# Optimization experiments

Measured on AMD Instinct MI355X. Metric: run time of the kernel, lower is better.

## Reference

```python
import jax, jax.numpy as jnp
import numpy as np

P = 3            # spline degree
N_KNOTS = 68     # len(t); K = N_KNOTS - P - 1 = 64
B, D_IN, D_OUT = 4096, 256, 256


def bspline_basis(u, t, p):
    """Vectorized Cox-de Boor recursion.
    u: (N,) evaluation points; t: (n,) sorted knot vector.
    Returns (N, n - p - 1) basis matrix.
    """
    n = t.shape[0]
    uu = u[:, None]                                   # (N, 1)
    # degree-0 indicators over half-open knot intervals: (N, n-1)
    Bmat = ((uu >= t[None, :-1]) & (uu < t[None, 1:])).astype(u.dtype)
    for d in range(1, p + 1):
        ld = t[d:n - 1] - t[:n - d - 1]               # (n-d-1,) left denominators
        rd = t[d + 1:] - t[1:n - d]                   # (n-d-1,) right denominators
        lt = jnp.where(ld > 0, (uu - t[None, :n - d - 1]) / jnp.where(ld > 0, ld, 1.0), 0.0)
        rt = jnp.where(rd > 0, (t[None, d + 1:] - uu) / jnp.where(rd > 0, rd, 1.0), 0.0)
        Bmat = lt * Bmat[:, :-1] + rt * Bmat[:, 1:]
    return Bmat                                        # (N, K)


def setup_inputs() -> dict:
    key = jax.random.key(0)
    k1, k2 = jax.random.split(key)
    K = N_KNOTS - P - 1
    x = jax.random.normal(k1, (B, D_IN), dtype=jnp.float32)
    coeffs = 0.01 * jax.random.normal(k2, (D_OUT, D_IN, K), dtype=jnp.float32)
    mask = jnp.ones((D_OUT, D_IN), dtype=jnp.float32)
    t = jnp.linspace(-4.0, 4.0, N_KNOTS, dtype=jnp.float32)
    return {"x": x, "coeffs": coeffs, "mask": mask, "t": t}


def reference(x, coeffs, mask, t):
    b, d_in = x.shape
    # basis for all (batch, input-dim) points at once -> (B, d_in, K)
    Bx = bspline_basis(x.reshape(-1), t, P).reshape(b, d_in, -1)
    C = coeffs * mask[..., None]                      # (d_out, d_in, K)
    y = jnp.einsum('bik,oik->bo', Bx, C)              # (B, d_out)
    return y
```

## Files before the change

kernel.cpp:

```cpp
#include <hip/hip_runtime.h>

#define NKNOTS 68
#define B_     4096
#define DIN    256
#define DOUT   256
#define KB_    64
#define BM     128
#define BN     128
#define LDT    72
#define KSPLIT 8

typedef unsigned short ushort_t;
typedef __bf16 bf16_t;
typedef bf16_t  bf16x8   __attribute__((ext_vector_type(8)));
typedef float   f32x4    __attribute__((ext_vector_type(4)));
typedef unsigned int u32x4 __attribute__((ext_vector_type(4)));
typedef ushort_t us16x4  __attribute__((ext_vector_type(4)));

__device__ __forceinline__ float bf2f(ushort_t b) {
    union { unsigned u; float f; } c; c.u = ((unsigned)b) << 16; return c.f;
}
__device__ __forceinline__ ushort_t f2bf(float f) {
    union { float f; unsigned u; } c; c.f = f;
    unsigned u = c.u;
    return (ushort_t)((u + 0x7FFFu + ((u >> 16) & 1u)) >> 16);
}
__device__ __forceinline__ bool is_fp32(const void* tkn) {
    return ((*(const unsigned*)tkn) & 0xFFFFu) == 0u;
}

__global__ void kan_maskmul(const void* __restrict__ coeffs,
                            const void* __restrict__ mask,
                            const void* __restrict__ tkn,
                            ushort_t* __restrict__ cp) {
    int tid = blockIdx.x * 256 + threadIdx.x;
    int oi = tid >> 3;
    int k8 = (tid & 7) * 8;
    size_t base = (size_t)oi * KB_ + k8;
    float v[8], m;
    if (is_fp32(tkn)) {
        const float* cf = (const float*)coeffs + base;
        f32x4 a = *(const f32x4*)cf;
        f32x4 b = *(const f32x4*)(cf + 4);
        v[0] = a.x; v[1] = a.y; v[2] = a.z; v[3] = a.w;
        v[4] = b.x; v[5] = b.y; v[6] = b.z; v[7] = b.w;
        m = ((const float*)mask)[oi];
    } else {
        const ushort_t* ch = (const ushort_t*)coeffs + base;
        u32x4 w = *(const u32x4*)ch;
        const ushort_t* h = (const ushort_t*)&w;
        #pragma unroll
        for (int e = 0; e < 8; ++e) v[e] = bf2f(h[e]);
        m = bf2f(((const ushort_t*)mask)[oi]);
    }
    us16x4 o0, o1;
    #pragma unroll
    for (int e = 0; e < 4; ++e) o0[e] = f2bf(v[e] * m);
    #pragma unroll
    for (int e = 0; e < 4; ++e) o1[e] = f2bf(v[4 + e] * m);
    *(us16x4*)(cp + base)     = o0;
    *(us16x4*)(cp + base + 4) = o1;
}

__global__ void kan_basis(const void* __restrict__ x,
                          const void* __restrict__ tkn,
                          ushort_t* __restrict__ basis4,
                          unsigned char* __restrict__ span) {
    __shared__ float tt[NKNOTS];
    int lt = threadIdx.x;
    bool f32 = is_fp32(tkn);
    if (lt < NKNOTS) tt[lt] = f32 ? ((const float*)tkn)[lt] : bf2f(((const ushort_t*)tkn)[lt]);
    __syncthreads();
    int g = blockIdx.x * 256 + lt;
    float u = f32 ? ((const float*)x)[g] : bf2f(((const ushort_t*)x)[g]);
    float N0 = 0.f, N1 = 0.f, N2 = 0.f, N3 = 0.f;
    int j = 0;
    bool valid = (u >= tt[0]) && (u < tt[NKNOTS - 1]);
    if (valid) {
        int lo = 0, hi = NKNOTS - 1;
        #pragma unroll
        for (int it = 0; it < 7; ++it) {
            int mid = (lo + hi) >> 1;
            if (u < tt[mid]) hi = mid; else lo = mid;
        }
        j = lo;
        float Nv[4];
        Nv[0] = 1.f; Nv[1] = 0.f; Nv[2] = 0.f; Nv[3] = 0.f;
        #pragma unroll
        for (int d = 1; d <= 3; ++d) {
            float saved = 0.f;
            #pragma unroll
            for (int r = 0; r < 3; ++r) {
                if (r < d) {
                    int il = j + r + 1 - d;
                    int ir = j + r + 1;
                    il = il < 0 ? 0 : (il > 67 ? 67 : il);
                    ir = ir > 67 ? 67 : ir;
                    float tl = tt[il], tr = tt[ir];
                    float denom = tr - tl;
                    float temp = (denom > 0.f) ? Nv[r] / denom : 0.f;
                    Nv[r] = saved + (tr - u) * temp;
                    saved = (u - tl) * temp;
                }
            }
            Nv[d] = saved;
        }
        N0 = Nv[0]; N1 = Nv[1]; N2 = Nv[2]; N3 = Nv[3];
    }
    int s = j - 3;
    int sc = s < 0 ? 0 : (s > 60 ? 60 : s);
    us16x4 o4;
    #pragma unroll
    for (int r = 0; r < 4; ++r) {
        int rr = (sc + r) - s;
        float v = 0.f;
        v = (rr == 0) ? N0 : v;
        v = (rr == 1) ? N1 : v;
        v = (rr == 2) ? N2 : v;
        v = (rr == 3) ? N3 : v;
        o4[r] = f2bf(v);
    }
    ((us16x4*)basis4)[g] = o4;
    span[g] = (unsigned char)sc;
}

__global__ __launch_bounds__(256, 2) void kan_gemm(
    const ushort_t* __restrict__ cp,
    const ushort_t* __restrict__ basis4,
    const unsigned char* __restrict__ span,
    float* __restrict__ part)
{
    __shared__ ushort_t smem[2 * BM * LDT];
    ushort_t* As = smem;
    ushort_t* Bs = smem + BM * LDT;

    int t  = threadIdx.x;
    int bx = blockIdx.x;
    int kt = bx & 7;
    int mt = (bx >> 3) & 31;
    int nt = bx >> 8;
    int b0 = mt * BM;
    int o0 = nt * BN;
    int i0 = kt * (DIN / KSPLIT);

    int wave = t >> 6;
    int lane = t & 63;
    int wm = (wave & 1) * 64;
    int wn = (wave >> 1) * 64;
    int l15 = lane & 15;
    int l4  = lane >> 4;

    f32x4 acc[4][4];
    #pragma unroll
    for (int a = 0; a < 4; ++a)
        #pragma unroll
        for (int b = 0; b < 4; ++b)
            acc[a][b] = (f32x4){0.f, 0.f, 0.f, 0.f};

    int zrow = t >> 2;
    int zq   = t & 3;
    int brow = t >> 1;
    int bh   = t & 1;

    for (int ii = 0; ii < DIN / KSPLIT; ++ii) {
        int i = i0 + ii;
        const u32x4* gB = (const u32x4*)(cp + ((size_t)(o0 + brow) * DIN + i) * KB_ + bh * 32);
        u32x4 vb0 = gB[0], vb1 = gB[1], vb2 = gB[2], vb3 = gB[3];
        int r0g = b0 + zrow, r1g = r0g + 64;
        unsigned s0 = span[(size_t)r0g * DIN + i];
        unsigned s1 = span[(size_t)r1g * DIN + i];
        ushort_t bv0 = basis4[((size_t)r0g * DIN + i) * 4 + zq];
        ushort_t bv1 = basis4[((size_t)r1g * DIN + i) * 4 + zq];
        u32x4 z4 = (u32x4){0u, 0u, 0u, 0u};
        u32x4* az0 = (u32x4*)(As + zrow * LDT + zq * 16);
        u32x4* az1 = (u32x4*)(As + (zrow + 64) * LDT + zq * 16);
        az0[0] = z4; az0[1] = z4;
        az1[0] = z4; az1[1] = z4;
        As[zrow * LDT + (int)s0 + zq] = bv0;
        As[(zrow + 64) * LDT + (int)s1 + zq] = bv1;
        u32x4* bw = (u32x4*)(Bs + brow * LDT + bh * 32);
        bw[0] = vb0; bw[1] = vb1; bw[2] = vb2; bw[3] = vb3;
        __syncthreads();
        #pragma unroll
        for (int ks = 0; ks < 2; ++ks) {
            bf16x8 af[4], bfr[4];
            #pragma unroll
            for (int a = 0; a < 4; ++a)
                af[a] = *(const bf16x8*)(As + (wm + a * 16 + l15) * LDT + ks * 32 + l4 * 8);
            #pragma unroll
            for (int b = 0; b < 4; ++b)
                bfr[b] = *(const bf16x8*)(Bs + (wn + b * 16 + l15) * LDT + ks * 32 + l4 * 8);
            #pragma unroll
            for (int a = 0; a < 4; ++a)
                #pragma unroll
                for (int b = 0; b < 4; ++b)
                    acc[a][b] = __builtin_amdgcn_mfma_f32_16x16x32_bf16(af[a], bfr[b], acc[a][b], 0, 0, 0);
        }
        __syncthreads();
    }
    float* pout = part + (size_t)kt * (B_ * DOUT);
    #pragma unroll
    for (int a = 0; a < 4; ++a) {
        int row_base = b0 + wm + a * 16 + l4 * 4;
        #pragma unroll
        for (int b = 0; b < 4; ++b) {
            int col = o0 + wn + b * 16 + l15;
            #pragma unroll
            for (int e = 0; e < 4; ++e)
                pout[(size_t)(row_base + e) * DOUT + col] = acc[a][b][e];
        }
    }
}

__global__ void kan_reduce(const float* __restrict__ part,
                           const void* __restrict__ tkn,
                           void* __restrict__ out) {
    int g = blockIdx.x * 256 + threadIdx.x;
    const f32x4* p4 = (const f32x4*)part;
    f32x4 s = p4[g];
    #pragma unroll
    for (int kt = 1; kt < KSPLIT; ++kt) {
        f32x4 v = p4[(size_t)kt * (B_ * DOUT / 4) + g];
        s.x += v.x; s.y += v.y; s.z += v.z; s.w += v.w;
    }
    if (is_fp32(tkn)) {
        ((f32x4*)out)[g] = s;
    } else {
        us16x4 o;
        o[0] = f2bf(s.x); o[1] = f2bf(s.y); o[2] = f2bf(s.z); o[3] = f2bf(s.w);
        ((us16x4*)out)[g] = o;
    }
}

extern "C" void kernel_launch(void* const* d_in, const int* in_sizes, int n_in,
                              void* d_out, int out_size, void* d_ws, size_t ws_size,
                              hipStream_t stream) {
    const void* x      = d_in[0];
    const void* coeffs = d_in[1];
    const void* mask   = d_in[2];
    const void* tkn    = d_in[3];

    char* ws = (char*)d_ws;
    ushort_t* cp            = (ushort_t*)(ws);
    ushort_t* basis4        = (ushort_t*)(ws + (8u  << 20));
    unsigned char* spanbuf  = (unsigned char*)(ws + (16u << 20));
    float* part             = (float*)(ws + (17u << 20));

    kan_maskmul<<<2048, 256, 0, stream>>>(coeffs, mask, tkn, cp);
    kan_basis<<<4096, 256, 0, stream>>>(x, tkn, basis4, spanbuf);
    kan_gemm<<<512, 256, 0, stream>>>(cp, basis4, spanbuf, part);
    kan_reduce<<<1024, 256, 0, stream>>>(part, tkn, d_out);
}
```

Baseline: 132.3 us.

## Fuse prep kernels, double split-K, use direct-to-LDS loads and bf16 partials

```diff
diff --git a/kernel.cpp b/kernel.cpp
--- a/kernel.cpp
+++ b/kernel.cpp
@@ -8,7 +8,8 @@
 #define BM     128
 #define BN     128
 #define LDT    72
-#define KSPLIT 8
+#define KSPLIT 16
+#define IPS    (DIN / KSPLIT)
 
 typedef unsigned short ushort_t;
 typedef __bf16 bf16_t;
@@ -17,6 +18,9 @@
 typedef unsigned int u32x4 __attribute__((ext_vector_type(4)));
 typedef ushort_t us16x4  __attribute__((ext_vector_type(4)));
 
+typedef __attribute__((address_space(1))) const unsigned int gu32;
+typedef __attribute__((address_space(3))) unsigned int lu32;
+
 __device__ __forceinline__ float bf2f(ushort_t b) {
     union { unsigned u; float f; } c; c.u = ((unsigned)b) << 16; return c.f;
 }
@@ -29,119 +33,119 @@
     return ((*(const unsigned*)tkn) & 0xFFFFu) == 0u;
 }
 
-__global__ void kan_maskmul(const void* __restrict__ coeffs,
-                            const void* __restrict__ mask,
-                            const void* __restrict__ tkn,
-                            ushort_t* __restrict__ cp) {
-    int tid = blockIdx.x * 256 + threadIdx.x;
-    int oi = tid >> 3;
-    int k8 = (tid & 7) * 8;
-    size_t base = (size_t)oi * KB_ + k8;
-    float v[8], m;
-    if (is_fp32(tkn)) {
-        const float* cf = (const float*)coeffs + base;
-        f32x4 a = *(const f32x4*)cf;
-        f32x4 b = *(const f32x4*)(cf + 4);
-        v[0] = a.x; v[1] = a.y; v[2] = a.z; v[3] = a.w;
-        v[4] = b.x; v[5] = b.y; v[6] = b.z; v[7] = b.w;
-        m = ((const float*)mask)[oi];
+__global__ void kan_prep(const void* __restrict__ coeffs,
+                         const void* __restrict__ mask,
+                         const void* __restrict__ x,
+                         const void* __restrict__ tkn,
+                         ushort_t* __restrict__ cp,
+                         ushort_t* __restrict__ basis4,
+                         unsigned char* __restrict__ span) {
+    __shared__ float tt[NKNOTS];
+    int blk = blockIdx.x;
+    int lt  = threadIdx.x;
+    bool f32 = is_fp32(tkn);
+
+    if (blk < 2048) {
+        int tid = blk * 256 + lt;
+        int oi = tid >> 3;
+        int k8 = (tid & 7) * 8;
+        size_t base = (size_t)oi * KB_ + k8;
+        float v[8], m;
+        if (f32) {
+            const float* cf = (const float*)coeffs + base;
+            f32x4 a = *(const f32x4*)cf;
+            f32x4 b = *(const f32x4*)(cf + 4);
+            v[0]=a.x; v[1]=a.y; v[2]=a.z; v[3]=a.w; v[4]=b.x; v[5]=b.y; v[6]=b.z; v[7]=b.w;
+            m = ((const float*)mask)[oi];
+        } else {
+            const ushort_t* ch = (const ushort_t*)coeffs + base;
+            u32x4 w = *(const u32x4*)ch;
+            const ushort_t* h = (const ushort_t*)&w;
+            #pragma unroll
+            for (int e = 0; e < 8; ++e) v[e] = bf2f(h[e]);
+            m = bf2f(((const ushort_t*)mask)[oi]);
+        }
+        us16x4 o0v, o1v;
+        #pragma unroll
+        for (int e = 0; e < 4; ++e) o0v[e] = f2bf(v[e] * m);
+        #pragma unroll
+        for (int e = 0; e < 4; ++e) o1v[e] = f2bf(v[4 + e] * m);
+        *(us16x4*)(cp + base)     = o0v;
+        *(us16x4*)(cp + base + 4) = o1v;
     } else {
-        const ushort_t* ch = (const ushort_t*)coeffs + base;
-        u32x4 w = *(const u32x4*)ch;
-        const ushort_t* h = (const ushort_t*)&w;
-        #pragma unroll
-        for (int e = 0; e < 8; ++e) v[e] = bf2f(h[e]);
-        m = bf2f(((const ushort_t*)mask)[oi]);
-    }
-    us16x4 o0, o1;
-    #pragma unroll
-    for (int e = 0; e < 4; ++e) o0[e] = f2bf(v[e] * m);
-    #pragma unroll
-    for (int e = 0; e < 4; ++e) o1[e] = f2bf(v[4 + e] * m);
-    *(us16x4*)(cp + base)     = o0;
-    *(us16x4*)(cp + base + 4) = o1;
-}
-
-__global__ void kan_basis(const void* __restrict__ x,
-                          const void* __restrict__ tkn,
-                          ushort_t* __restrict__ basis4,
-                          unsigned char* __restrict__ span) {
-    __shared__ float tt[NKNOTS];
-    int lt = threadIdx.x;
-    bool f32 = is_fp32(tkn);
-    if (lt < NKNOTS) tt[lt] = f32 ? ((const float*)tkn)[lt] : bf2f(((const ushort_t*)tkn)[lt]);
-    __syncthreads();
-    int g = blockIdx.x * 256 + lt;
-    float u = f32 ? ((const float*)x)[g] : bf2f(((const ushort_t*)x)[g]);
-    float N0 = 0.f, N1 = 0.f, N2 = 0.f, N3 = 0.f;
-    int j = 0;
-    bool valid = (u >= tt[0]) && (u < tt[NKNOTS - 1]);
-    if (valid) {
-        int lo = 0, hi = NKNOTS - 1;
-        #pragma unroll
-        for (int it = 0; it < 7; ++it) {
-            int mid = (lo + hi) >> 1;
-            if (u < tt[mid]) hi = mid; else lo = mid;
-        }
-        j = lo;
-        float Nv[4];
-        Nv[0] = 1.f; Nv[1] = 0.f; Nv[2] = 0.f; Nv[3] = 0.f;
-        #pragma unroll
-        for (int d = 1; d <= 3; ++d) {
-            float saved = 0.f;
-            #pragma unroll
-            for (int r = 0; r < 3; ++r) {
-                if (r < d) {
-                    int il = j + r + 1 - d;
-                    int ir = j + r + 1;
-                    il = il < 0 ? 0 : (il > 67 ? 67 : il);
-                    ir = ir > 67 ? 67 : ir;
-                    float tl = tt[il], tr = tt[ir];
-                    float denom = tr - tl;
-                    float temp = (denom > 0.f) ? Nv[r] / denom : 0.f;
-                    Nv[r] = saved + (tr - u) * temp;
-                    saved = (u - tl) * temp;
+        if (lt < NKNOTS) tt[lt] = f32 ? ((const float*)tkn)[lt] : bf2f(((const ushort_t*)tkn)[lt]);
+        __syncthreads();
+        int g = (blk - 2048) * 256 + lt;
+        float u = f32 ? ((const float*)x)[g] : bf2f(((const ushort_t*)x)[g]);
+        float N0 = 0.f, N1 = 0.f, N2 = 0.f, N3 = 0.f;
+        int j = 0;
+        bool valid = (u >= tt[0]) && (u < tt[NKNOTS - 1]);
+        if (valid) {
+            int lo = 0, hi = NKNOTS - 1;
+            #pragma unroll
+            for (int it = 0; it < 7; ++it) {
+                int mid = (lo + hi) >> 1;
+                if (u < tt[mid]) hi = mid; else lo = mid;
+            }
+            j = lo;
+            float Nv[4];
+            Nv[0] = 1.f; Nv[1] = 0.f; Nv[2] = 0.f; Nv[3] = 0.f;
+            #pragma unroll
+            for (int d = 1; d <= 3; ++d) {
+                float saved = 0.f;
+                #pragma unroll
+                for (int r = 0; r < 3; ++r) {
+                    if (r < d) {
+                        int il = j + r + 1 - d;
+                        int ir = j + r + 1;
+                        il = il < 0 ? 0 : (il > 67 ? 67 : il);
+                        ir = ir > 67 ? 67 : ir;
+                        float tl = tt[il], tr = tt[ir];
+                        float denom = tr - tl;
+                        float temp = (denom > 0.f) ? Nv[r] / denom : 0.f;
+                        Nv[r] = saved + (tr - u) * temp;
+                        saved = (u - tl) * temp;
+                    }
                 }
+                Nv[d] = saved;
             }
-            Nv[d] = saved;
-        }
-        N0 = Nv[0]; N1 = Nv[1]; N2 = Nv[2]; N3 = Nv[3];
-    }
-    int s = j - 3;
-    int sc = s < 0 ? 0 : (s > 60 ? 60 : s);
-    us16x4 o4;
-    #pragma unroll
-    for (int r = 0; r < 4; ++r) {
-        int rr = (sc + r) - s;
-        float v = 0.f;
-        v = (rr == 0) ? N0 : v;
-        v = (rr == 1) ? N1 : v;
-        v = (rr == 2) ? N2 : v;
-        v = (rr == 3) ? N3 : v;
-        o4[r] = f2bf(v);
-    }
-    ((us16x4*)basis4)[g] = o4;
-    span[g] = (unsigned char)sc;
-}
-
-__global__ __launch_bounds__(256, 2) void kan_gemm(
+            N0 = Nv[0]; N1 = Nv[1]; N2 = Nv[2]; N3 = Nv[3];
+        }
+        int s = j - 3;
+        int sc = s < 0 ? 0 : (s > 60 ? 60 : s);
+        us16x4 o4;
+        #pragma unroll
+        for (int r = 0; r < 4; ++r) {
+            int rr = (sc + r) - s;
+            float v = 0.f;
+            v = (rr == 0) ? N0 : v;
+            v = (rr == 1) ? N1 : v;
+            v = (rr == 2) ? N2 : v;
+            v = (rr == 3) ? N3 : v;
+            o4[r] = f2bf(v);
+        }
+        ((us16x4*)basis4)[g] = o4;
+        span[g] = (unsigned char)sc;
+    }
+}
+
+__global__ __launch_bounds__(256, 4) void kan_gemm(
     const ushort_t* __restrict__ cp,
     const ushort_t* __restrict__ basis4,
     const unsigned char* __restrict__ span,
-    float* __restrict__ part)
+    ushort_t* __restrict__ part)
 {
-    __shared__ ushort_t smem[2 * BM * LDT];
-    ushort_t* As = smem;
-    ushort_t* Bs = smem + BM * LDT;
+    __shared__ __align__(16) ushort_t As[BM * LDT];
+    __shared__ __align__(16) ushort_t Bs[BM * KB_];
 
     int t  = threadIdx.x;
     int bx = blockIdx.x;
-    int kt = bx & 7;
-    int mt = (bx >> 3) & 31;
-    int nt = bx >> 8;
+    int kt = bx & (KSPLIT - 1);
+    int mt = (bx >> 4) & 31;
+    int nt = bx >> 9;
     int b0 = mt * BM;
     int o0 = nt * BN;
-    int i0 = kt * (DIN / KSPLIT);
+    int i0 = kt * IPS;
 
     int wave = t >> 6;
     int lane = t & 63;
@@ -150,6 +154,13 @@
     int l15 = lane & 15;
     int l4  = lane >> 4;
 
+    {
+        unsigned* As32 = (unsigned*)As;
+        #pragma unroll
+        for (int j = 0; j < (BM * LDT / 2) / 256; ++j) As32[t + j * 256] = 0u;
+    }
+    __syncthreads();
+
     f32x4 acc[4][4];
     #pragma unroll
     for (int a = 0; a < 4; ++a)
@@ -159,27 +170,30 @@
 
     int zrow = t >> 2;
     int zq   = t & 3;
-    int brow = t >> 1;
-    int bh   = t & 1;
-
-    for (int ii = 0; ii < DIN / KSPLIT; ++ii) {
+    int last0 = 0, last1 = 0;
+
+    for (int ii = 0; ii < IPS; ++ii) {
         int i = i0 + ii;
-        const u32x4* gB = (const u32x4*)(cp + ((size_t)(o0 + brow) * DIN + i) * KB_ + bh * 32);
-        u32x4 vb0 = gB[0], vb1 = gB[1], vb2 = gB[2], vb3 = gB[3];
-        int r0g = b0 + zrow, r1g = r0g + 64;
-        unsigned s0 = span[(size_t)r0g * DIN + i];
-        unsigned s1 = span[(size_t)r1g * DIN + i];
-        ushort_t bv0 = basis4[((size_t)r0g * DIN + i) * 4 + zq];
-        ushort_t bv1 = basis4[((size_t)r1g * DIN + i) * 4 + zq];
-        u32x4 z4 = (u32x4){0u, 0u, 0u, 0u};
-        u32x4* az0 = (u32x4*)(As + zrow * LDT + zq * 16);
-        u32x4* az1 = (u32x4*)(As + (zrow + 64) * LDT + zq * 16);
-        az0[0] = z4; az0[1] = z4;
-        az1[0] = z4; az1[1] = z4;
-        As[zrow * LDT + (int)s0 + zq] = bv0;
-        As[(zrow + 64) * LDT + (int)s1 + zq] = bv1;
-        u32x4* bw = (u32x4*)(Bs + brow * LDT + bh * 32);
-        bw[0] = vb0; bw[1] = vb1; bw[2] = vb2; bw[3] = vb3;
+        size_t gi0 = (size_t)(b0 + zrow) * DIN + i;
+        size_t gi1 = (size_t)(b0 + zrow + 64) * DIN + i;
+        int s0 = span[gi0];
+        int s1 = span[gi1];
+        ushort_t bv0 = basis4[gi0 * 4 + zq];
+        ushort_t bv1 = basis4[gi1 * 4 + zq];
+        #pragma unroll
+        for (int j = 0; j < 4; ++j) {
+            int slot = wave * 256 + j * 64 + lane;
+            int row  = slot >> 3;
+            int c    = (slot & 7) ^ (row & 7);
+            const ushort_t* g = cp + ((size_t)(o0 + row) * DIN + i) * KB_ + c * 8;
+            lu32* l = (lu32*)(Bs + (wave * 256 + j * 64) * 8);
+            __builtin_amdgcn_global_load_lds((gu32*)g, l, 16, 0, 0);
+        }
+        As[zrow * LDT + last0 + zq] = 0;
+        As[(zrow + 64) * LDT + last1 + zq] = 0;
+        As[zrow * LDT + s0 + zq] = bv0;
+        As[(zrow + 64) * LDT + s1 + zq] = bv1;
+        last0 = s0; last1 = s1;
         __syncthreads();
         #pragma unroll
         for (int ks = 0; ks < 2; ++ks) {
@@ -188,8 +202,11 @@
             for (int a = 0; a < 4; ++a)
                 af[a] = *(const bf16x8*)(As + (wm + a * 16 + l15) * LDT + ks * 32 + l4 * 8);
             #pragma unroll
-            for (int b = 0; b < 4; ++b)
-                bfr[b] = *(const bf16x8*)(Bs + (wn + b * 16 + l15) * LDT + ks * 32 + l4 * 8);
+            for (int b = 0; b < 4; ++b) {
+                int brow = wn + b * 16 + l15;
+                int c2 = (ks * 4 + l4) ^ (brow & 7);
+                bfr[b] = *(const bf16x8*)(Bs + brow * KB_ + c2 * 8);
+            }
             #pragma unroll
             for (int a = 0; a < 4; ++a)
                 #pragma unroll
@@ -198,7 +215,7 @@
         }
         __syncthreads();
     }
-    float* pout = part + (size_t)kt * (B_ * DOUT);
+    ushort_t* pout = part + (size_t)kt * (B_ * DOUT);
     #pragma unroll
     for (int a = 0; a < 4; ++a) {
         int row_base = b0 + wm + a * 16 + l4 * 4;
@@ -207,21 +224,21 @@
             int col = o0 + wn + b * 16 + l15;
             #pragma unroll
             for (int e = 0; e < 4; ++e)
-                pout[(size_t)(row_base + e) * DOUT + col] = acc[a][b][e];
-        }
-    }
-}
-
-__global__ void kan_reduce(const float* __restrict__ part,
+                pout[(size_t)(row_base + e) * DOUT + col] = f2bf(acc[a][b][e]);
+        }
+    }
+}
+
+__global__ void kan_reduce(const ushort_t* __restrict__ part,
                            const void* __restrict__ tkn,
                            void* __restrict__ out) {
     int g = blockIdx.x * 256 + threadIdx.x;
-    const f32x4* p4 = (const f32x4*)part;
-    f32x4 s = p4[g];
+    const us16x4* p4 = (const us16x4*)part;
+    f32x4 s = (f32x4){0.f, 0.f, 0.f, 0.f};
     #pragma unroll
-    for (int kt = 1; kt < KSPLIT; ++kt) {
-        f32x4 v = p4[(size_t)kt * (B_ * DOUT / 4) + g];
-        s.x += v.x; s.y += v.y; s.z += v.z; s.w += v.w;
+    for (int kt = 0; kt < KSPLIT; ++kt) {
+        us16x4 v = p4[(size_t)kt * (B_ * DOUT / 4) + g];
+        s.x += bf2f(v[0]); s.y += bf2f(v[1]); s.z += bf2f(v[2]); s.w += bf2f(v[3]);
     }
     if (is_fp32(tkn)) {
         ((f32x4*)out)[g] = s;
@@ -244,10 +261,9 @@
     ushort_t* cp            = (ushort_t*)(ws);
     ushort_t* basis4        = (ushort_t*)(ws + (8u  << 20));
     unsigned char* spanbuf  = (unsigned char*)(ws + (16u << 20));
-    float* part             = (float*)(ws + (17u << 20));
-
-    kan_maskmul<<<2048, 256, 0, stream>>>(coeffs, mask, tkn, cp);
-    kan_basis<<<4096, 256, 0, stream>>>(x, tkn, basis4, spanbuf);
-    kan_gemm<<<512, 256, 0, stream>>>(cp, basis4, spanbuf, part);
+    ushort_t* part          = (ushort_t*)(ws + (17u << 20));
+
+    kan_prep<<<6144, 256, 0, stream>>>(coeffs, mask, x, tkn, cp, basis4, spanbuf);
+    kan_gemm<<<1024, 256, 0, stream>>>(cp, basis4, spanbuf, part);
     kan_reduce<<<1024, 256, 0, stream>>>(part, tkn, d_out);
 }
```

After: 118.6 us. -10.3%, faster.
